# Kernel optimization log

Hardware: AMD Instinct MI355X
Metric: run time of the kernel (lower is better)

## Reference

```python
import jax, jax.numpy as jnp
import numpy as np

B, IN_CH, OUT_CH, STYLE_DIM, K, H, W = 16, 512, 512, 512, 3, 32, 32


def setup_inputs() -> dict:
    key = jax.random.key(0)
    k1, k2, k3, k4 = jax.random.split(key, 4)
    return {
        "x": jax.random.normal(k1, (B, IN_CH, H, W), dtype=jnp.float32),
        "style": jax.random.normal(k2, (B, STYLE_DIM), dtype=jnp.float32),
        "aff_weight": jax.random.normal(k3, (IN_CH, STYLE_DIM), dtype=jnp.float32),
        "aff_bias": jnp.zeros((IN_CH,), dtype=jnp.float32),
        "conv_weight": jax.random.normal(k4, (OUT_CH, IN_CH, K, K), dtype=jnp.float32),
    }


def reference(x, style, aff_weight, aff_bias, conv_weight):
    # EqualizedLinearAct with act='linear': y = style @ (W*scale)^T + bias
    style_dim = aff_weight.shape[1]
    aff_scale = 1.0 / np.sqrt(style_dim)  # gain=1.0
    s = style @ (aff_weight * aff_scale).T + aff_bias + 1.0  # [B, in]

    out_ch, in_ch, k, _ = conv_weight.shape
    w_scale = 1.0 / np.sqrt(in_ch * k * k)  # gain / sqrt(in*k*k)
    # per-sample modulated weights: [B, out, in, k, k]
    w = conv_weight[None, :, :, :, :] * s[:, None, :, None, None] * w_scale
    # demodulation
    d = jax.lax.rsqrt(jnp.sum(w * w, axis=(2, 3, 4), keepdims=True) + 1e-8)
    w = w * d

    # groups=B grouped conv == per-sample conv; up=1, flip_weight=True ->
    # plain cross-correlation (same as torch F.conv2d / lax conv default).
    def conv1(xi, wi):
        # xi: [in, H, W], wi: [out, in, k, k]
        return jax.lax.conv_general_dilated(
            xi[None], wi, window_strides=(1, 1), padding="SAME",
            dimension_numbers=("NCHW", "OIHW", "NCHW"))[0]

    return jax.vmap(conv1)(x, w)  # [B, out, H, W]
```

## Files before the change

kernel.cpp:

```cpp
#include <hip/hip_runtime.h>


#define BATCH   16
#define CIN     512
#define COUT    512
#define IMG     32
#define PAD_IMG 34

static constexpr float AFF_SCALE = 0.044194173824159216f;
static constexpr float W_SCALE   = 0.014731391274719739f;

typedef __bf16 bf16x8 __attribute__((ext_vector_type(8)));
typedef float  f32x4  __attribute__((ext_vector_type(4)));

__device__ inline unsigned short f2bf(float f) {
    union { float f; unsigned int u; } v; v.f = f;
    unsigned int u = v.u;
    unsigned int r = (u + 0x7FFFu + ((u >> 16) & 1u)) >> 16;
    return (unsigned short)r;
}

__device__ inline float waveReduceSum(float v) {
    #pragma unroll
    for (int off = 32; off > 0; off >>= 1) v += __shfl_xor(v, off, 64);
    return v;
}

__global__ void prep1(const float* __restrict__ cw,
                      const float* __restrict__ style,
                      const float* __restrict__ aw,
                      const float* __restrict__ ab,
                      unsigned short* __restrict__ w_t,
                      float* __restrict__ wsq,
                      float* __restrict__ s_out) {
    const int tid = threadIdx.x;
    if (blockIdx.x < 1024) {
        __shared__ float wl[2304];
        const float* src = cw + (size_t)blockIdx.x * 2304;
        for (int j = tid; j < 2304; j += 256) wl[j] = src[j];
        __syncthreads();
        const int idx = blockIdx.x * 256 + tid;
        const int base = tid * 9;
        float acc = 0.f;
        #pragma unroll
        for (int e = 0; e < 9; ++e) {
            float v = wl[base + e];
            acc += v * v;
            w_t[e * (COUT * CIN) + idx] = f2bf(v);
        }
        wsq[idx] = acc;
    } else {
        const int q = blockIdx.x - 1024;
        const int b = q >> 7;
        const int i = (q & 127) * 4 + (tid >> 6);
        const int lane = tid & 63;
        float sum = 0.f;
        #pragma unroll
        for (int k = 0; k < 512; k += 64)
            sum += style[b * 512 + k + lane] * aw[i * 512 + k + lane];
        sum = waveReduceSum(sum);
        if (lane == 0)
            s_out[b * 512 + i] = sum * AFF_SCALE + ab[i] + 1.0f;
    }
}

__global__ void prep2(const float* __restrict__ x,
                      const float* __restrict__ s_in,
                      const float* __restrict__ wsq,
                      unsigned short* __restrict__ xpad,
                      float* __restrict__ scl) {
    const int tid = threadIdx.x;
    if (blockIdx.x >= 4352) {
        const int q = blockIdx.x - 4352;
        const int b = q >> 7;
        const int o = (q & 127) * 4 + (tid >> 6);
        const int lane = tid & 63;
        float sum = 0.f;
        #pragma unroll
        for (int i = 0; i < 512; i += 64) {
            float sv = s_in[b * 512 + i + lane];
            sum += sv * sv * wsq[o * 512 + i + lane];
        }
        sum = waveReduceSum(sum);
        if (lane == 0)
            scl[b * 512 + o] = W_SCALE * rsqrtf(W_SCALE * W_SCALE * sum + 1e-8f);
        return;
    }
    const int c0   = blockIdx.x & 7;
    const int rest = blockIdx.x >> 3;
    const int hh   = rest % 34;
    const int b    = rest / 34;
    const int c0b  = c0 * 64;
    unsigned short* rowbase = xpad + (((size_t)b * PAD_IMG + hh) * PAD_IMG) * 512;

    if (hh == 0 || hh == PAD_IMG - 1) {
        for (int j = tid; j < 34 * 32; j += 256) {
            int ww = j >> 5, cp = (j & 31) * 2;
            *(unsigned int*)(rowbase + (size_t)ww * 512 + c0b + cp) = 0u;
        }
        return;
    }

    __shared__ float t[64][33];
    const int h = hh - 1;
    {
        const int wx = tid & 31;
        const int cb = (tid >> 5) * 8;
        const float* xb = x + (((size_t)b * 512 + c0b + cb) * IMG + h) * IMG + wx;
        #pragma unroll
        for (int j = 0; j < 8; ++j)
            t[cb + j][wx] = xb[(size_t)j * (IMG * IMG)] * s_in[b * 512 + c0b + cb + j];
    }
    __syncthreads();
    {
        const int p  = tid >> 3;
        const int cc = (tid & 7) * 8;
        unsigned short* dst = rowbase + (size_t)(p + 1) * 512 + c0b + cc;
        uint4 pk;
        pk.x = (unsigned)f2bf(t[cc + 0][p]) | ((unsigned)f2bf(t[cc + 1][p]) << 16);
        pk.y = (unsigned)f2bf(t[cc + 2][p]) | ((unsigned)f2bf(t[cc + 3][p]) << 16);
        pk.z = (unsigned)f2bf(t[cc + 4][p]) | ((unsigned)f2bf(t[cc + 5][p]) << 16);
        pk.w = (unsigned)f2bf(t[cc + 6][p]) | ((unsigned)f2bf(t[cc + 7][p]) << 16);
        *(uint4*)dst = pk;
    }
    if (tid < 64) {
        int ww = (tid >> 5) ? (PAD_IMG - 1) : 0;
        int cp = (tid & 31) * 2;
        *(unsigned int*)(rowbase + (size_t)ww * 512 + c0b + cp) = 0u;
    }
}


#define SYNC() do {                                                           \
    asm volatile("s_waitcnt lgkmcnt(0)" ::: "memory");                        \
    __builtin_amdgcn_s_barrier();                                             \
    __builtin_amdgcn_sched_barrier(0);                                        \
} while (0)

#define LOADSTEP(stp) do {                                                    \
    const int e_  = (stp) >> 3;                                               \
    const int kc_ = ((stp) & 7) << 6;                                         \
    const int kh_ = (e_ * 11) >> 5;                                           \
    const int kw_ = e_ - kh_ * 3;                                             \
    const unsigned short* Ab_ = wt + (size_t)e_ * (COUT * CIN)                \
                                   + (size_t)m0 * 512 + kc_;                  \
    const unsigned short* Bb_ = xpad + bImgBase                               \
                              + (size_t)((h0 + kh_) * PAD_IMG + kw_) * 512    \
                              + kc_;                                          \
    ra0 = *(const uint4*)(Ab_ + aOff0);                                       \
    ra1 = *(const uint4*)(Ab_ + aOff1);                                       \
    rb0 = *(const uint4*)(Bb_ + bOff0);                                       \
    rb1 = *(const uint4*)(Bb_ + bOff1);                                       \
    rb2 = *(const uint4*)(Bb_ + bOff2);                                       \
    rb3 = *(const uint4*)(Bb_ + bOff3);                                       \
} while (0)

#define COMMIT(Albuf, Blbuf) do {                                             \
    *(uint4*)((Albuf) + lA0) = ra0;                                           \
    *(uint4*)((Albuf) + lA1) = ra1;                                           \
    *(uint4*)((Blbuf) + lB0) = rb0;                                           \
    *(uint4*)((Blbuf) + lB1) = rb1;                                           \
    *(uint4*)((Blbuf) + lB2) = rb2;                                           \
    *(uint4*)((Blbuf) + lB3) = rb3;                                           \
} while (0)

__global__ __launch_bounds__(512, 2) void conv_mfma(
    const unsigned short* __restrict__ wt,
    const unsigned short* __restrict__ xpad,
    const float* __restrict__ scl,
    float* __restrict__ out)
{
    __shared__ __align__(16) unsigned char smem[98304];
    unsigned short* Alds0 = (unsigned short*)(smem);
    unsigned short* Alds1 = (unsigned short*)(smem + 16384);
    unsigned short* Blds0 = (unsigned short*)(smem + 32768);
    unsigned short* Blds1 = (unsigned short*)(smem + 65536);
    __shared__ float sclds[128];

    const int tid = threadIdx.x;
    const int id    = blockIdx.x;
    const int xcd   = id & 7;
    const int local = id >> 3;
    const int gp    = xcd * 8 + (local >> 2);
    const int m0  = (local & 3) * 128;
    const int b   = gp >> 2;
    const int h0  = (gp & 3) * 8;

    if (tid < 128) sclds[tid] = scl[b * 512 + m0 + tid];

    const int wid  = tid >> 6;
    const int lane = tid & 63;
    const int wm = (wid >> 1) & 1;
    const int wn = wid & 1;
    const int kg = wid >> 2;

    const f32x4 vzero = {0.f, 0.f, 0.f, 0.f};
    f32x4 acc[4][8];
    #pragma unroll
    for (int i = 0; i < 4; ++i)
        #pragma unroll
        for (int j = 0; j < 8; ++j) acc[i][j] = vzero;

    int aOff0, aOff1, lA0, lA1;
    int bOff0, bOff1, bOff2, bOff3, lB0, lB1, lB2, lB3;
    {
        int f, row, c, p;
        f = tid;              row = f >> 3; c = f & 7; p = c ^ (row & 7);
        aOff0 = row * 512 + c * 8;  lA0 = row * 64 + p * 8;
        f = 512 + tid;        row = f >> 3; c = f & 7; p = c ^ (row & 7);
        aOff1 = row * 512 + c * 8;  lA1 = row * 64 + p * 8;

        f = tid;              row = f >> 3; c = f & 7; p = c ^ (row & 7);
        bOff0 = ((row >> 5) * PAD_IMG + (row & 31)) * 512 + c * 8;
        lB0 = row * 64 + p * 8;
        f = 512 + tid;        row = f >> 3; c = f & 7; p = c ^ (row & 7);
        bOff1 = ((row >> 5) * PAD_IMG + (row & 31)) * 512 + c * 8;
        lB1 = row * 64 + p * 8;
        f = 1024 + tid;       row = f >> 3; c = f & 7; p = c ^ (row & 7);
        bOff2 = ((row >> 5) * PAD_IMG + (row & 31)) * 512 + c * 8;
        lB2 = row * 64 + p * 8;
        f = 1536 + tid;       row = f >> 3; c = f & 7; p = c ^ (row & 7);
        bOff3 = ((row >> 5) * PAD_IMG + (row & 31)) * 512 + c * 8;
        lB3 = row * 64 + p * 8;
    }

    const size_t bImgBase = (size_t)b * PAD_IMG * PAD_IMG * 512;

    uint4 ra0, ra1, rb0, rb1, rb2, rb3;

    LOADSTEP(0);

    const int rl   = lane & 15;
    const int kch  = lane >> 4;
    const int swz  = ((kg * 4 + kch) ^ (rl & 7)) * 8;
    const int arow = (wm * 64 + rl) * 64;
    const int brow = (wn * 128 + rl) * 64;

    for (int step = 0; step < 72; ++step) {
        unsigned short* Ab_lds = (step & 1) ? Alds1 : Alds0;
        unsigned short* Bb_lds = (step & 1) ? Blds1 : Blds0;
        COMMIT(Ab_lds, Bb_lds);
        const int nxt = step + 1 < 72 ? step + 1 : 71;
        LOADSTEP(nxt);
        SYNC();

        bf16x8 af[4], bfr[8];
        #pragma unroll
        for (int mi = 0; mi < 4; ++mi)
            af[mi] = *(const bf16x8*)(Ab_lds + arow + mi * (16 * 64) + swz);
        bfr[0] = *(const bf16x8*)(Bb_lds + brow + 0 * (16 * 64) + swz);
        __builtin_amdgcn_s_setprio(1);
        #pragma unroll
        for (int ni = 0; ni < 8; ++ni) {
            if (ni < 7)
                bfr[ni + 1] =
                    *(const bf16x8*)(Bb_lds + brow + (ni + 1) * (16 * 64) + swz);
            #pragma unroll
            for (int mi = 0; mi < 4; ++mi)
                acc[mi][ni] = __builtin_amdgcn_mfma_f32_16x16x32_bf16(
                    af[mi], bfr[ni], acc[mi][ni], 0, 0, 0);
        }
        __builtin_amdgcn_s_setprio(0);
    }

    const int colp = lane & 15;
    const int rowq = (lane >> 4) * 4;
    float* ep = (float*)smem;
    float* reg = ep + wn * 8192;
    for (int wmr = 0; wmr < 2; ++wmr) {
        __syncthreads();
        if (wm == wmr && kg == 1) {
            #pragma unroll
            for (int mi = 0; mi < 4; ++mi)
                #pragma unroll
                for (int ni = 0; ni < 8; ++ni)
                    *(f32x4*)(reg + ((mi * 8 + ni) * 64 + lane) * 4) =
                        acc[mi][ni];
        }
        __syncthreads();
        if (wm == wmr && kg == 0) {
            #pragma unroll
            for (int mi = 0; mi < 4; ++mi) {
                #pragma unroll
                for (int ni = 0; ni < 8; ++ni) {
                    const f32x4 o =
                        *(const f32x4*)(reg + ((mi * 8 + ni) * 64 + lane) * 4);
                    const int p = h0 * 32 + wn * 128 + ni * 16 + colp;
                    #pragma unroll
                    for (int r2 = 0; r2 < 4; ++r2) {
                        const int ol = wm * 64 + mi * 16 + rowq + r2;
                        out[(((size_t)b * 512 + m0 + ol) << 10) + p] =
                            (acc[mi][ni][r2] + o[r2]) * sclds[ol];
                    }
                }
            }
        }
    }
}

extern "C" void kernel_launch(void* const* d_in, const int* in_sizes, int n_in,
                              void* d_out, int out_size, void* d_ws, size_t ws_size,
                              hipStream_t stream) {
    const float* x     = (const float*)d_in[0];
    const float* style = (const float*)d_in[1];
    const float* aw    = (const float*)d_in[2];
    const float* ab    = (const float*)d_in[3];
    const float* cw    = (const float*)d_in[4];
    float* out = (float*)d_out;

    char* ws = (char*)d_ws;
    float* s_buf          = (float*)(ws);
    float* scl            = (float*)(ws + 32768);
    float* wsq            = (float*)(ws + 65536);
    unsigned short* w_t   = (unsigned short*)(ws + 1114112);
    unsigned short* x_pad = (unsigned short*)(ws + 5832704);

    prep1<<<dim3(3072), 256, 0, stream>>>(cw, style, aw, ab, w_t, wsq, s_buf);
    prep2<<<dim3(6400), 256, 0, stream>>>(x, s_buf, wsq, x_pad, scl);
    conv_mfma<<<dim3(256), 512, 0, stream>>>(w_t, x_pad, scl, out);
}
```

Before: 171.4 us.

## Vectorize prep kernel loads/stores and add MFMA schedule group barriers

The prep kernels now use float4 global loads and packed bf16 pair stores. The weight transpose block handles two weight rows per thread, so the launch uses half as many weight blocks. The x scaling/transposing pass now loads float4 rows, and the style/demod dot products read float4. The conv main loop adds sched_group_barrier hints to interleave LDS reads with MFMAs. These aim to cut memory instruction count in prep and improve MFMA/LDS overlap in the GEMM, at the risk of forcing the compiler's schedule and possibly hurting it.

```diff
diff --git a/kernel.cpp b/kernel.cpp
--- a/kernel.cpp
+++ b/kernel.cpp
@@ -34,30 +34,39 @@
                       float* __restrict__ wsq,
                       float* __restrict__ s_out) {
     const int tid = threadIdx.x;
-    if (blockIdx.x < 1024) {
-        __shared__ float wl[2304];
-        const float* src = cw + (size_t)blockIdx.x * 2304;
-        for (int j = tid; j < 2304; j += 256) wl[j] = src[j];
+    if (blockIdx.x < 512) {
+        __shared__ float wl[4608];
+        const float* src = cw + (size_t)blockIdx.x * 4608;
+        for (int j = tid; j < 1152; j += 256)
+            *(float4*)(wl + j * 4) = *(const float4*)(src + j * 4);
         __syncthreads();
-        const int idx = blockIdx.x * 256 + tid;
-        const int base = tid * 9;
-        float acc = 0.f;
+        const int idx0 = blockIdx.x * 512 + tid * 2;
+        const int base = tid * 18;
+        float acc0 = 0.f, acc1 = 0.f;
         #pragma unroll
         for (int e = 0; e < 9; ++e) {
-            float v = wl[base + e];
-            acc += v * v;
-            w_t[e * (COUT * CIN) + idx] = f2bf(v);
-        }
-        wsq[idx] = acc;
+            float v0 = wl[base + e];
+            float v1 = wl[base + 9 + e];
+            acc0 += v0 * v0;
+            acc1 += v1 * v1;
+            unsigned int pk = (unsigned)f2bf(v0) | ((unsigned)f2bf(v1) << 16);
+            *(unsigned int*)(w_t + (size_t)e * (COUT * CIN) + idx0) = pk;
+        }
+        *(float2*)(wsq + idx0) = make_float2(acc0, acc1);
     } else {
-        const int q = blockIdx.x - 1024;
+        const int q = blockIdx.x - 512;
         const int b = q >> 7;
         const int i = (q & 127) * 4 + (tid >> 6);
         const int lane = tid & 63;
+        const float4* a4 = (const float4*)(aw + (size_t)i * 512);
+        const float4* s4 = (const float4*)(style + (size_t)b * 512);
         float sum = 0.f;
         #pragma unroll
-        for (int k = 0; k < 512; k += 64)
-            sum += style[b * 512 + k + lane] * aw[i * 512 + k + lane];
+        for (int r = 0; r < 2; ++r) {
+            float4 av = a4[lane * 2 + r];
+            float4 sv = s4[lane * 2 + r];
+            sum += av.x * sv.x + av.y * sv.y + av.z * sv.z + av.w * sv.w;
+        }
         sum = waveReduceSum(sum);
         if (lane == 0)
             s_out[b * 512 + i] = sum * AFF_SCALE + ab[i] + 1.0f;
@@ -75,11 +84,15 @@
         const int b = q >> 7;
         const int o = (q & 127) * 4 + (tid >> 6);
         const int lane = tid & 63;
+        const float4* w4p = (const float4*)(wsq + (size_t)o * 512);
+        const float4* s4p = (const float4*)(s_in + (size_t)b * 512);
         float sum = 0.f;
         #pragma unroll
-        for (int i = 0; i < 512; i += 64) {
-            float sv = s_in[b * 512 + i + lane];
-            sum += sv * sv * wsq[o * 512 + i + lane];
+        for (int r = 0; r < 2; ++r) {
+            float4 wv = w4p[lane * 2 + r];
+            float4 sv = s4p[lane * 2 + r];
+            sum += sv.x * sv.x * wv.x + sv.y * sv.y * wv.y
+                 + sv.z * sv.z * wv.z + sv.w * sv.w * wv.w;
         }
         sum = waveReduceSum(sum);
         if (lane == 0)
@@ -103,13 +116,18 @@
 
     __shared__ float t[64][33];
     const int h = hh - 1;
-    {
-        const int wx = tid & 31;
-        const int cb = (tid >> 5) * 8;
-        const float* xb = x + (((size_t)b * 512 + c0b + cb) * IMG + h) * IMG + wx;
-        #pragma unroll
-        for (int j = 0; j < 8; ++j)
-            t[cb + j][wx] = xb[(size_t)j * (IMG * IMG)] * s_in[b * 512 + c0b + cb + j];
+    #pragma unroll
+    for (int r = 0; r < 2; ++r) {
+        const int f   = r * 256 + tid;
+        const int chl = f >> 3;
+        const int w4  = (f & 7) * 4;
+        float4 xv = *(const float4*)(
+            x + (((size_t)b * 512 + c0b + chl) * IMG + h) * IMG + w4);
+        const float sv = s_in[b * 512 + c0b + chl];
+        t[chl][w4 + 0] = xv.x * sv;
+        t[chl][w4 + 1] = xv.y * sv;
+        t[chl][w4 + 2] = xv.z * sv;
+        t[chl][w4 + 3] = xv.w * sv;
     }
     __syncthreads();
     {
@@ -249,6 +267,7 @@
         for (int mi = 0; mi < 4; ++mi)
             af[mi] = *(const bf16x8*)(Ab_lds + arow + mi * (16 * 64) + swz);
         bfr[0] = *(const bf16x8*)(Bb_lds + brow + 0 * (16 * 64) + swz);
+        __builtin_amdgcn_sched_group_barrier(0x100, 5, 0);
         __builtin_amdgcn_s_setprio(1);
         #pragma unroll
         for (int ni = 0; ni < 8; ++ni) {
@@ -259,6 +278,9 @@
             for (int mi = 0; mi < 4; ++mi)
                 acc[mi][ni] = __builtin_amdgcn_mfma_f32_16x16x32_bf16(
                     af[mi], bfr[ni], acc[mi][ni], 0, 0, 0);
+            if (ni < 7)
+                __builtin_amdgcn_sched_group_barrier(0x100, 1, 0);
+            __builtin_amdgcn_sched_group_barrier(0x008, 4, 0);
         }
         __builtin_amdgcn_s_setprio(0);
     }
@@ -315,7 +337,7 @@
     unsigned short* w_t   = (unsigned short*)(ws + 1114112);
     unsigned short* x_pad = (unsigned short*)(ws + 5832704);
 
-    prep1<<<dim3(3072), 256, 0, stream>>>(cw, style, aw, ab, w_t, wsq, s_buf);
+    prep1<<<dim3(2560), 256, 0, stream>>>(cw, style, aw, ab, w_t, wsq, s_buf);
     prep2<<<dim3(6400), 256, 0, stream>>>(x, s_buf, wsq, x_pad, scl);
     conv_mfma<<<dim3(256), 512, 0, stream>>>(w_t, x_pad, scl, out);
 }
```

Result: no change. 171.2 us (-0.1%).
